# Optimization experiments

Measured on AMD Instinct MI355X. Metric: run time of the kernel, lower is better.

Reference implementation:

```python
import jax, jax.numpy as jnp
import numpy as np

A, B, D, H, O = 64, 4096, 50, 192, 3

def _xavier(key, shape, gain=0.5):
    fan_in, fan_out = shape[-1], shape[-2]
    limit = gain * np.sqrt(6.0 / (fan_in + fan_out))
    return jax.random.uniform(key, shape, jnp.float32, -limit, limit)

def setup_inputs() -> dict:
    key = jax.random.key(0)
    ks = jax.random.split(key, 12)
    return {
        "x": jax.random.normal(ks[0], (B, D), jnp.float32),
        "input_norm_weight": _xavier(ks[1], (A, D)),
        "input_norm_bias": jnp.zeros((A, D), jnp.float32),
        "layer1_weight": _xavier(ks[2], (A, H, D)),
        "layer1_bias": jnp.zeros((A, H), jnp.float32),
        "layer2_weight": _xavier(ks[3], (A, H, H)),
        "layer2_bias": jnp.zeros((A, H), jnp.float32),
        "layer3_weight": _xavier(ks[4], (A, H, H)),
        "layer3_bias": jnp.zeros((A, H), jnp.float32),
        "output_weight": _xavier(ks[5], (A, O, H)),
        "output_bias": jnp.zeros((A, O), jnp.float32),
        "skip1_weight": _xavier(ks[6], (A, H, D)),
        "skip1_bias": jnp.zeros((A, H), jnp.float32),
        "skip2_weight": _xavier(ks[7], (A, H, H)),
        "skip2_bias": jnp.zeros((A, H), jnp.float32),
        "hidden_norm_weight": _xavier(ks[8], (A, H)),
        "hidden_norm_bias": jnp.zeros((A, H), jnp.float32),
    }

def reference(x, input_norm_weight, input_norm_bias,
              layer1_weight, layer1_bias, layer2_weight, layer2_bias,
              layer3_weight, layer3_bias, output_weight, output_bias,
              skip1_weight, skip1_bias, skip2_weight, skip2_bias,
              hidden_norm_weight, hidden_norm_bias):
    # NOTE: the vectorized ensemble's "norms" are affine-only (no mean/var), per source.
    # x: [B, D] -> broadcast over agents: [A, B, D]
    x_norm = x[None, :, :] * input_norm_weight[:, None, :] + input_norm_bias[:, None, :]
    gelu = lambda t: jax.nn.gelu(t, approximate=False)  # torch F.gelu exact
    # per-agent GEMMs: [A,B,in] x [A,out,in] -> [A,B,out]
    h1 = gelu(jnp.einsum('abi,ahi->abh', x_norm, layer1_weight) + layer1_bias[:, None, :]) \
         + jnp.einsum('abi,ahi->abh', x_norm, skip1_weight) + skip1_bias[:, None, :]
    h2 = gelu(jnp.einsum('abi,ahi->abh', h1, layer2_weight) + layer2_bias[:, None, :]) \
         + jnp.einsum('abi,ahi->abh', h1, skip2_weight) + skip2_bias[:, None, :]
    h3 = jnp.einsum('abi,ahi->abh', h2, layer3_weight) + layer3_bias[:, None, :] + h2
    h3 = h3 * hidden_norm_weight[:, None, :] + hidden_norm_bias[:, None, :]
    logits = jnp.einsum('abh,aoh->abo', h3, output_weight) + output_bias[:, None, :]
    return logits  # [A, B, O]
```

## Files before the change

### kernel.cpp

```cpp
#include <hip/hip_runtime.h>
#include <math.h>

#define A_N 64
#define B_N 4096
#define D_N 50
#define H_N 192
#define O_N 3

typedef __attribute__((ext_vector_type(8))) __bf16 bf16x8;
typedef __attribute__((ext_vector_type(4))) float f32x4;

#define W1_OFF   0
#define S1_OFF   786432
#define W2_OFF   1572864
#define S2_OFF   3932160
#define W3_OFF   6291456
#define OW_OFF   8650752
#define WS_ELEMS 8847360

#if __has_builtin(__builtin_amdgcn_rcpf)
#define FRCP(x) __builtin_amdgcn_rcpf(x)
#else
#define FRCP(x) (1.0f / (x))
#endif
#if __has_builtin(__builtin_amdgcn_exp2f)
#define FEXP2(x) __builtin_amdgcn_exp2f(x)
#else
#define FEXP2(x) exp2f(x)
#endif

__device__ __forceinline__ float gelu_f(float xx) {
    float t  = 0.70710678118654752440f * xx;
    float at = fabsf(t);
    float k  = FRCP(fmaf(0.3275911f, at, 1.0f));
    float p  = fmaf(k, 1.061405429f, -1.453152027f);
    p = fmaf(k, p, 1.421413741f);
    p = fmaf(k, p, -0.284496736f);
    p = fmaf(k, p, 0.254829592f);
    p = p * k;
    float e  = FEXP2(t * t * -1.44269504088896340736f);
    float er = fmaf(-p, e, 1.0f);
    er = (t < 0.f) ? -er : er;
    return 0.5f * xx * (1.0f + er);
}

__global__ void prep_kernel(const float* __restrict__ w1, const float* __restrict__ s1,
                            const float* __restrict__ w2, const float* __restrict__ s2,
                            const float* __restrict__ w3, const float* __restrict__ ow,
                            __bf16* __restrict__ ws) {
    int idx8 = blockIdx.x * 256 + threadIdx.x;
    if (idx8 >= WS_ELEMS / 8) return;
    int idx = idx8 * 8;
    bf16x8 v;
    if (idx < W2_OFF) {
        const float* src = (idx < S1_OFF) ? w1 : s1;
        int r = (idx < S1_OFF) ? idx : idx - S1_OFF;
        int a = r / 12288;  r %= 12288;
        int nt = r / 1024;  r %= 1024;
        int ks = r / 512;   r %= 512;
        int lane = r >> 3;
        int n = nt * 16 + (lane & 15);
        int k = ks * 32 + (lane >> 4) * 8;
        const float* p = src + (size_t)(a * H_N + n) * D_N + k;
        #pragma unroll
        for (int j = 0; j < 8; ++j)
            v[j] = (k + j < D_N) ? (__bf16)p[j] : (__bf16)0.f;
    } else if (idx < OW_OFF) {
        int r = idx - W2_OFF;
        const float* src = w2;
        if (r >= 4718592)      { src = w3; r -= 4718592; }
        else if (r >= 2359296) { src = s2; r -= 2359296; }
        int a = r / 36864;  r %= 36864;
        int nt = r / 3072;  r %= 3072;
        int ks = r / 512;   r %= 512;
        int lane = r >> 3;
        int n = nt * 16 + (lane & 15);
        int k = ks * 32 + (lane >> 4) * 8;
        const float* p = src + (size_t)(a * H_N + n) * H_N + k;
        f32x4 f0 = *(const f32x4*)p;
        f32x4 f1 = *(const f32x4*)(p + 4);
        #pragma unroll
        for (int j = 0; j < 4; ++j) { v[j] = (__bf16)f0[j]; v[4 + j] = (__bf16)f1[j]; }
    } else {
        int r = idx - OW_OFF;
        int a = r / 3072;   r %= 3072;
        int ks = r / 512;   r %= 512;
        int lane = r >> 3;
        int n = lane & 15;
        int k = ks * 32 + (lane >> 4) * 8;
        if (n < O_N) {
            const float* p = ow + (size_t)(a * O_N + n) * H_N + k;
            f32x4 f0 = *(const f32x4*)p;
            f32x4 f1 = *(const f32x4*)(p + 4);
            #pragma unroll
            for (int j = 0; j < 4; ++j) { v[j] = (__bf16)f0[j]; v[4 + j] = (__bf16)f1[j]; }
        } else {
            #pragma unroll
            for (int j = 0; j < 8; ++j) v[j] = (__bf16)0.f;
        }
    }
    *(bf16x8*)(ws + idx) = v;
}

#define MFMA(a, b, c) __builtin_amdgcn_mfma_f32_16x16x32_bf16((a), (b), (c), 0, 0, 0)

__global__ __launch_bounds__(256, 2)
void srek_mfma(const float* __restrict__ x,
               const float* __restrict__ inw, const float* __restrict__ inb,
               const float* __restrict__ b1,  const float* __restrict__ b2,
               const float* __restrict__ b3,  const float* __restrict__ s1b,
               const float* __restrict__ s2b, const float* __restrict__ hnw,
               const float* __restrict__ hnb, const float* __restrict__ ob,
               const __bf16* __restrict__ ws, float* __restrict__ out) {
    __shared__ __bf16 Xs[64 * 72];
    __shared__ __bf16 Hs[64 * 200];
    __shared__ __bf16 Bs[24 * 512];

    const int bid  = blockIdx.x;
    const int slot = bid >> 3;
    const int tile = slot & 63;
    const int a    = ((bid & 7) << 3) | (slot >> 6);
    const int row0 = tile * 64;

    const int tid  = threadIdx.x;
    const int lane = tid & 63;
    const int wv   = tid >> 6;
    const int ln   = lane & 15;
    const int quad = lane >> 4;
    const int aH   = a * H_N;
    const int c0   = wv * 48;
    const int l8   = lane * 8;
    const int f6   = wv * 6;
    const int f3   = wv * 3;

    const __bf16* W1 = ws + W1_OFF + a * 12288;
    const __bf16* S1 = ws + S1_OFF + a * 12288;
    const __bf16* W2 = ws + W2_OFF + a * 36864;
    const __bf16* S2 = ws + S2_OFF + a * 36864;
    const __bf16* W3 = ws + W3_OFF + a * 36864;
    const __bf16* OWp= ws + OW_OFF + a * 3072;

    bf16x8 pf[6];
    f32x4 accT[12], accS[12], h2f[12];
    const f32x4 zero = {0.f, 0.f, 0.f, 0.f};

    #pragma unroll
    for (int i = 0; i < 6; ++i) {
        int f = f6 + i; int nt = f % 12;
        const __bf16* base = (f < 12) ? W1 : S1;
        pf[i] = *(const bf16x8*)(base + (nt * 2 + 0) * 512 + l8);
    }

    for (int e = tid; e < 64 * 64; e += 256) {
        int r = e >> 6, k = e & 63;
        float v = 0.f;
        if (k < D_N) v = x[(size_t)(row0 + r) * D_N + k] * inw[a * D_N + k] + inb[a * D_N + k];
        Xs[r * 72 + k] = (__bf16)v;
    }

    auto stage24 = [&]() {
        #pragma unroll
        for (int i = 0; i < 6; ++i) *(bf16x8*)(Bs + (f6 + i) * 512 + l8) = pf[i];
    };
    auto stage12 = [&]() {
        #pragma unroll
        for (int i = 0; i < 3; ++i) *(bf16x8*)(Bs + (f3 + i) * 512 + l8) = pf[i];
    };
    auto pf24 = [&](const __bf16* Wb, const __bf16* Sb, int KS, int ks) {
        #pragma unroll
        for (int i = 0; i < 6; ++i) {
            int f = f6 + i; int nt = f % 12;
            const __bf16* base = (f < 12) ? Wb : Sb;
            pf[i] = *(const bf16x8*)(base + (nt * KS + ks) * 512 + l8);
        }
    };
    auto pf12 = [&](int ks) {
        #pragma unroll
        for (int i = 0; i < 3; ++i)
            pf[i] = *(const bf16x8*)(W3 + ((f3 + i) * 6 + ks) * 512 + l8);
    };
    auto compute_dual = [&](const __bf16* As, int pitch, int ks) {
        bf16x8 bw[3], bs2[3];
        #pragma unroll
        for (int t = 0; t < 3; ++t) {
            bw[t]  = *(const bf16x8*)(Bs + (wv * 3 + t) * 512 + l8);
            bs2[t] = *(const bf16x8*)(Bs + (12 + wv * 3 + t) * 512 + l8);
        }
        #pragma unroll
        for (int mt = 0; mt < 4; ++mt) {
            bf16x8 av = *(const bf16x8*)(As + (mt * 16 + ln) * pitch + ks * 32 + quad * 8);
            #pragma unroll
            for (int t = 0; t < 3; ++t) {
                accT[mt * 3 + t] = MFMA(av, bw[t],  accT[mt * 3 + t]);
                accS[mt * 3 + t] = MFMA(av, bs2[t], accS[mt * 3 + t]);
            }
        }
    };
    auto compute_single = [&](int ks) {
        bf16x8 bw[3];
        #pragma unroll
        for (int t = 0; t < 3; ++t)
            bw[t] = *(const bf16x8*)(Bs + (wv * 3 + t) * 512 + l8);
        #pragma unroll
        for (int mt = 0; mt < 4; ++mt) {
            bf16x8 av = *(const bf16x8*)(Hs + (mt * 16 + ln) * 200 + ks * 32 + quad * 8);
            #pragma unroll
            for (int t = 0; t < 3; ++t)
                accT[mt * 3 + t] = MFMA(av, bw[t], accT[mt * 3 + t]);
        }
    };

    #pragma unroll
    for (int i = 0; i < 12; ++i) { accT[i] = zero; accS[i] = zero; }

    stage24();
    pf24(W1, S1, 2, 1);
    __syncthreads();
    compute_dual(Xs, 72, 0);
    __syncthreads();
    stage24();
    pf24(W2, S2, 6, 0);
    __syncthreads();
    compute_dual(Xs, 72, 1);

    #pragma unroll
    for (int t = 0; t < 3; ++t) {
        int col = c0 + t * 16 + ln;
        float bb = b1[aH + col], sb = s1b[aH + col];
        #pragma unroll
        for (int mt = 0; mt < 4; ++mt) {
            f32x4 vT = accT[mt * 3 + t], vS = accS[mt * 3 + t];
            #pragma unroll
            for (int rg = 0; rg < 4; ++rg) {
                float v = gelu_f(vT[rg] + bb) + vS[rg] + sb;
                Hs[(mt * 16 + quad * 4 + rg) * 200 + col] = (__bf16)v;
            }
        }
    }
    #pragma unroll
    for (int i = 0; i < 12; ++i) { accT[i] = zero; accS[i] = zero; }
    __syncthreads();
    stage24();
    pf24(W2, S2, 6, 1);
    __syncthreads();

    #pragma unroll 1
    for (int ks = 0; ks < 5; ++ks) {
        compute_dual(Hs, 200, ks);
        __syncthreads();
        stage24();
        if (ks < 4) pf24(W2, S2, 6, ks + 2);
        else        pf12(0);
        __syncthreads();
    }
    compute_dual(Hs, 200, 5);
    #pragma unroll
    for (int t = 0; t < 3; ++t) {
        int col = c0 + t * 16 + ln;
        float bb = b2[aH + col], sb = s2b[aH + col];
        #pragma unroll
        for (int mt = 0; mt < 4; ++mt) {
            #pragma unroll
            for (int rg = 0; rg < 4; ++rg)
                h2f[mt * 3 + t][rg] = gelu_f(accT[mt * 3 + t][rg] + bb) + accS[mt * 3 + t][rg] + sb;
        }
    }
    #pragma unroll
    for (int i = 0; i < 12; ++i) accT[i] = zero;
    __syncthreads();
    stage12();
    #pragma unroll
    for (int t = 0; t < 3; ++t) {
        int col = c0 + t * 16 + ln;
        #pragma unroll
        for (int mt = 0; mt < 4; ++mt)
            #pragma unroll
            for (int rg = 0; rg < 4; ++rg)
                Hs[(mt * 16 + quad * 4 + rg) * 200 + col] = (__bf16)h2f[mt * 3 + t][rg];
    }
    pf12(1);
    __syncthreads();

    #pragma unroll 1
    for (int ks = 0; ks < 5; ++ks) {
        compute_single(ks);
        __syncthreads();
        stage12();
        if (ks < 4) pf12(ks + 2);
        __syncthreads();
    }
    compute_single(5);

    bf16x8 owf[6];
    #pragma unroll
    for (int ks = 0; ks < 6; ++ks)
        owf[ks] = *(const bf16x8*)(OWp + ks * 512 + l8);

    #pragma unroll
    for (int t = 0; t < 3; ++t) {
        int col = c0 + t * 16 + ln;
        float b3v = b3[aH + col], nw = hnw[aH + col], nb = hnb[aH + col];
        #pragma unroll
        for (int mt = 0; mt < 4; ++mt)
            #pragma unroll
            for (int rg = 0; rg < 4; ++rg)
                h2f[mt * 3 + t][rg] = (accT[mt * 3 + t][rg] + b3v + h2f[mt * 3 + t][rg]) * nw + nb;
    }
    __syncthreads();
    #pragma unroll
    for (int t = 0; t < 3; ++t) {
        int col = c0 + t * 16 + ln;
        #pragma unroll
        for (int mt = 0; mt < 4; ++mt)
            #pragma unroll
            for (int rg = 0; rg < 4; ++rg)
                Hs[(mt * 16 + quad * 4 + rg) * 200 + col] = (__bf16)h2f[mt * 3 + t][rg];
    }
    __syncthreads();

    {
        f32x4 acco = zero;
        #pragma unroll
        for (int ks = 0; ks < 6; ++ks) {
            bf16x8 av = *(const bf16x8*)(Hs + (wv * 16 + ln) * 200 + ks * 32 + quad * 8);
            acco = MFMA(av, owf[ks], acco);
        }
        if (ln < O_N) {
            float obv = ob[a * O_N + ln];
            #pragma unroll
            for (int rg = 0; rg < 4; ++rg) {
                int r = row0 + wv * 16 + quad * 4 + rg;
                out[((size_t)a * B_N + r) * O_N + ln] = acco[rg] + obv;
            }
        }
    }
}

extern "C" void kernel_launch(void* const* d_in, const int* in_sizes, int n_in,
                              void* d_out, int out_size, void* d_ws, size_t ws_size,
                              hipStream_t stream) {
    const float* x   = (const float*)d_in[0];
    const float* inw = (const float*)d_in[1];
    const float* inb = (const float*)d_in[2];
    const float* w1  = (const float*)d_in[3];
    const float* b1  = (const float*)d_in[4];
    const float* w2  = (const float*)d_in[5];
    const float* b2  = (const float*)d_in[6];
    const float* w3  = (const float*)d_in[7];
    const float* b3  = (const float*)d_in[8];
    const float* ow  = (const float*)d_in[9];
    const float* ob  = (const float*)d_in[10];
    const float* s1w = (const float*)d_in[11];
    const float* s1b = (const float*)d_in[12];
    const float* s2w = (const float*)d_in[13];
    const float* s2b = (const float*)d_in[14];
    const float* hnw = (const float*)d_in[15];
    const float* hnb = (const float*)d_in[16];

    __bf16* ws = (__bf16*)d_ws;

    prep_kernel<<<dim3((WS_ELEMS / 8 + 255) / 256), dim3(256), 0, stream>>>(
        w1, s1w, w2, s2w, w3, ow, ws);

    srek_mfma<<<dim3(A_N * (B_N / 64)), dim3(256), 0, stream>>>(
        x, inw, inb, b1, b2, b3, s1b, s2b, hnw, hnb, ob, ws, (float*)d_out);
}
```

Before: 263.1 us.

## Load weight fragments straight to registers, drop LDS staging, transpose MFMA operands

The main kernel no longer stages weight fragments through shared memory. Each wave loads its own pre-swizzled bf16 weight fragments from global memory into registers one k-step ahead, which removes most of the per-k-step __syncthreads barriers. MFMA operands are swapped so each lane's output holds 4 consecutive columns, which allows vectorized bias loads and bf16x4 stores into shared memory. The prep kernel is rewritten to transpose tiles through shared memory with coalesced reads, and occupancy is raised to 3 blocks per CU. The trade-offs are more register pressure and repeated global weight reads by the four waves.

```diff
diff --git a/kernel.cpp b/kernel.cpp
--- a/kernel.cpp
+++ b/kernel.cpp
@@ -8,6 +8,7 @@
 #define O_N 3
 
 typedef __attribute__((ext_vector_type(8))) __bf16 bf16x8;
+typedef __attribute__((ext_vector_type(4))) __bf16 bf16x4;
 typedef __attribute__((ext_vector_type(4))) float f32x4;
 
 #define W1_OFF   0
@@ -44,67 +45,89 @@
     return 0.5f * xx * (1.0f + er);
 }
 
-__global__ void prep_kernel(const float* __restrict__ w1, const float* __restrict__ s1,
-                            const float* __restrict__ w2, const float* __restrict__ s2,
-                            const float* __restrict__ w3, const float* __restrict__ ow,
-                            __bf16* __restrict__ ws) {
-    int idx8 = blockIdx.x * 256 + threadIdx.x;
-    if (idx8 >= WS_ELEMS / 8) return;
-    int idx = idx8 * 8;
-    bf16x8 v;
-    if (idx < W2_OFF) {
-        const float* src = (idx < S1_OFF) ? w1 : s1;
-        int r = (idx < S1_OFF) ? idx : idx - S1_OFF;
-        int a = r / 12288;  r %= 12288;
-        int nt = r / 1024;  r %= 1024;
-        int ks = r / 512;   r %= 512;
-        int lane = r >> 3;
-        int n = nt * 16 + (lane & 15);
-        int k = ks * 32 + (lane >> 4) * 8;
-        const float* p = src + (size_t)(a * H_N + n) * D_N + k;
-        #pragma unroll
-        for (int j = 0; j < 8; ++j)
-            v[j] = (k + j < D_N) ? (__bf16)p[j] : (__bf16)0.f;
-    } else if (idx < OW_OFF) {
-        int r = idx - W2_OFF;
-        const float* src = w2;
-        if (r >= 4718592)      { src = w3; r -= 4718592; }
-        else if (r >= 2359296) { src = s2; r -= 2359296; }
-        int a = r / 36864;  r %= 36864;
-        int nt = r / 3072;  r %= 3072;
-        int ks = r / 512;   r %= 512;
-        int lane = r >> 3;
-        int n = nt * 16 + (lane & 15);
-        int k = ks * 32 + (lane >> 4) * 8;
-        const float* p = src + (size_t)(a * H_N + n) * H_N + k;
-        f32x4 f0 = *(const f32x4*)p;
-        f32x4 f1 = *(const f32x4*)(p + 4);
-        #pragma unroll
-        for (int j = 0; j < 4; ++j) { v[j] = (__bf16)f0[j]; v[4 + j] = (__bf16)f1[j]; }
+__global__ __launch_bounds__(256)
+void prep_kernel(const float* __restrict__ w1, const float* __restrict__ s1,
+                 const float* __restrict__ w2, const float* __restrict__ s2,
+                 const float* __restrict__ w3, const float* __restrict__ ow,
+                 __bf16* __restrict__ ws) {
+    __shared__ __bf16 T[192 * 72];
+    const int b   = blockIdx.x;
+    const int tid = threadIdx.x;
+
+    if (b < 384) {
+        int m = b / 128;
+        int r = b % 128; int a = r >> 1; int half = r & 1;
+        const float* src = ((m == 0) ? w2 : (m == 1) ? s2 : w3) + (size_t)a * 36864;
+        __bf16* dst = ws + ((m == 0) ? W2_OFF : (m == 1) ? S2_OFF : W3_OFF) + (size_t)a * 36864;
+        for (int rc = half * 3; rc < half * 3 + 3; ++rc) {
+            #pragma unroll
+            for (int i = 0; i < 6; ++i) {
+                int f4 = i * 256 + tid;
+                int row = f4 / 48, kc = (f4 % 48) * 4;
+                f32x4 v = *(const f32x4*)(src + (size_t)(rc * 32 + row) * 192 + kc);
+                bf16x4 o;
+                #pragma unroll
+                for (int j = 0; j < 4; ++j) o[j] = (__bf16)v[j];
+                *(bf16x4*)(T + row * 200 + kc) = o;
+            }
+            __syncthreads();
+            #pragma unroll
+            for (int i = 0; i < 3; ++i) {
+                int fr = i * 256 + tid;
+                int f = fr >> 6, lane = fr & 63;
+                int ntl = f / 6, ks = f % 6;
+                int n = ntl * 16 + (lane & 15), k = ks * 32 + (lane >> 4) * 8;
+                bf16x8 v = *(const bf16x8*)(T + n * 200 + k);
+                *(bf16x8*)(dst + ((size_t)(rc * 2 + ntl) * 6 + ks) * 512 + lane * 8) = v;
+            }
+            __syncthreads();
+        }
+    } else if (b < 512) {
+        int r = b - 384; int m = r >> 6; int a = r & 63;
+        const float* src = (m ? s1 : w1) + (size_t)a * 9600;
+        __bf16* dst = ws + (m ? S1_OFF : W1_OFF) + (size_t)a * 12288;
+        for (int e = tid; e < 192 * 72; e += 256) T[e] = (__bf16)0.f;
+        __syncthreads();
+        for (int e = tid; e < 9600; e += 256) {
+            int row = e / 50, k = e - row * 50;
+            T[row * 72 + k] = (__bf16)src[e];
+        }
+        __syncthreads();
+        #pragma unroll
+        for (int i = 0; i < 6; ++i) {
+            int fr = i * 256 + tid;
+            int f = fr >> 6, lane = fr & 63;
+            int nt = f >> 1, ks = f & 1;
+            int n = nt * 16 + (lane & 15), k = ks * 32 + (lane >> 4) * 8;
+            bf16x8 v = *(const bf16x8*)(T + n * 72 + k);
+            *(bf16x8*)(dst + (size_t)(nt * 2 + ks) * 512 + lane * 8) = v;
+        }
     } else {
-        int r = idx - OW_OFF;
-        int a = r / 3072;   r %= 3072;
-        int ks = r / 512;   r %= 512;
-        int lane = r >> 3;
-        int n = lane & 15;
-        int k = ks * 32 + (lane >> 4) * 8;
-        if (n < O_N) {
-            const float* p = ow + (size_t)(a * O_N + n) * H_N + k;
-            f32x4 f0 = *(const f32x4*)p;
-            f32x4 f1 = *(const f32x4*)(p + 4);
-            #pragma unroll
-            for (int j = 0; j < 4; ++j) { v[j] = (__bf16)f0[j]; v[4 + j] = (__bf16)f1[j]; }
-        } else {
-            #pragma unroll
-            for (int j = 0; j < 8; ++j) v[j] = (__bf16)0.f;
-        }
-    }
-    *(bf16x8*)(ws + idx) = v;
+        int r = b - 512;
+        #pragma unroll
+        for (int i = 0; i < 8; ++i) {
+            int fr = (r * 8 + i) * 256 + tid;
+            int a = fr / 384, rem = fr - a * 384;
+            int ks = rem >> 6, lane = rem & 63;
+            int n = lane & 15, k = ks * 32 + (lane >> 4) * 8;
+            bf16x8 v;
+            if (n < O_N) {
+                const float* p = ow + ((size_t)a * O_N + n) * H_N + k;
+                f32x4 f0 = *(const f32x4*)p, f1 = *(const f32x4*)(p + 4);
+                #pragma unroll
+                for (int j = 0; j < 4; ++j) { v[j] = (__bf16)f0[j]; v[4 + j] = (__bf16)f1[j]; }
+            } else {
+                #pragma unroll
+                for (int j = 0; j < 8; ++j) v[j] = (__bf16)0.f;
+            }
+            *(bf16x8*)(ws + OW_OFF + (size_t)a * 3072 + ks * 512 + lane * 8) = v;
+        }
+    }
 }
 
 #define MFMA(a, b, c) __builtin_amdgcn_mfma_f32_16x16x32_bf16((a), (b), (c), 0, 0, 0)
 
-__global__ __launch_bounds__(256, 2)
+__global__ __launch_bounds__(256, 3)
 void srek_mfma(const float* __restrict__ x,
                const float* __restrict__ inw, const float* __restrict__ inb,
                const float* __restrict__ b1,  const float* __restrict__ b2,
@@ -114,7 +137,6 @@
                const __bf16* __restrict__ ws, float* __restrict__ out) {
     __shared__ __bf16 Xs[64 * 72];
     __shared__ __bf16 Hs[64 * 200];
-    __shared__ __bf16 Bs[24 * 512];
 
     const int bid  = blockIdx.x;
     const int slot = bid >> 3;
@@ -130,25 +152,23 @@
     const int aH   = a * H_N;
     const int c0   = wv * 48;
     const int l8   = lane * 8;
-    const int f6   = wv * 6;
     const int f3   = wv * 3;
 
-    const __bf16* W1 = ws + W1_OFF + a * 12288;
-    const __bf16* S1 = ws + S1_OFF + a * 12288;
-    const __bf16* W2 = ws + W2_OFF + a * 36864;
-    const __bf16* S2 = ws + S2_OFF + a * 36864;
-    const __bf16* W3 = ws + W3_OFF + a * 36864;
-    const __bf16* OWp= ws + OW_OFF + a * 3072;
-
-    bf16x8 pf[6];
+    const __bf16* W1 = ws + W1_OFF + (size_t)a * 12288;
+    const __bf16* S1 = ws + S1_OFF + (size_t)a * 12288;
+    const __bf16* W2 = ws + W2_OFF + (size_t)a * 36864;
+    const __bf16* S2 = ws + S2_OFF + (size_t)a * 36864;
+    const __bf16* W3 = ws + W3_OFF + (size_t)a * 36864;
+    const __bf16* OWp= ws + OW_OFF + (size_t)a * 3072;
+
+    bf16x8 nxt[6];
     f32x4 accT[12], accS[12], h2f[12];
     const f32x4 zero = {0.f, 0.f, 0.f, 0.f};
 
     #pragma unroll
-    for (int i = 0; i < 6; ++i) {
-        int f = f6 + i; int nt = f % 12;
-        const __bf16* base = (f < 12) ? W1 : S1;
-        pf[i] = *(const bf16x8*)(base + (nt * 2 + 0) * 512 + l8);
+    for (int t = 0; t < 3; ++t) {
+        nxt[t]     = *(const bf16x8*)(W1 + ((f3 + t) * 2 + 0) * 512 + l8);
+        nxt[3 + t] = *(const bf16x8*)(S1 + ((f3 + t) * 2 + 0) * 512 + l8);
     }
 
     for (int e = tid; e < 64 * 64; e += 256) {
@@ -158,163 +178,155 @@
         Xs[r * 72 + k] = (__bf16)v;
     }
 
-    auto stage24 = [&]() {
-        #pragma unroll
-        for (int i = 0; i < 6; ++i) *(bf16x8*)(Bs + (f6 + i) * 512 + l8) = pf[i];
+    auto compute_dual = [&](const __bf16* As, int pitch, int ks,
+                            const bf16x8* cw, const bf16x8* cs) {
+        #pragma unroll
+        for (int mt = 0; mt < 4; ++mt) {
+            bf16x8 av = *(const bf16x8*)(As + (mt * 16 + ln) * pitch + ks * 32 + quad * 8);
+            #pragma unroll
+            for (int t = 0; t < 3; ++t) {
+                accT[mt * 3 + t] = MFMA(cw[t], av, accT[mt * 3 + t]);
+                accS[mt * 3 + t] = MFMA(cs[t], av, accS[mt * 3 + t]);
+            }
+        }
     };
-    auto stage12 = [&]() {
-        #pragma unroll
-        for (int i = 0; i < 3; ++i) *(bf16x8*)(Bs + (f3 + i) * 512 + l8) = pf[i];
+    auto compute_single = [&](int ks, const bf16x8* cw) {
+        #pragma unroll
+        for (int mt = 0; mt < 4; ++mt) {
+            bf16x8 av = *(const bf16x8*)(Hs + (mt * 16 + ln) * 200 + ks * 32 + quad * 8);
+            #pragma unroll
+            for (int t = 0; t < 3; ++t)
+                accT[mt * 3 + t] = MFMA(cw[t], av, accT[mt * 3 + t]);
+        }
     };
-    auto pf24 = [&](const __bf16* Wb, const __bf16* Sb, int KS, int ks) {
-        #pragma unroll
-        for (int i = 0; i < 6; ++i) {
-            int f = f6 + i; int nt = f % 12;
-            const __bf16* base = (f < 12) ? Wb : Sb;
-            pf[i] = *(const bf16x8*)(base + (nt * KS + ks) * 512 + l8);
-        }
-    };
-    auto pf12 = [&](int ks) {
-        #pragma unroll
-        for (int i = 0; i < 3; ++i)
-            pf[i] = *(const bf16x8*)(W3 + ((f3 + i) * 6 + ks) * 512 + l8);
-    };
-    auto compute_dual = [&](const __bf16* As, int pitch, int ks) {
-        bf16x8 bw[3], bs2[3];
+
+    #pragma unroll
+    for (int i = 0; i < 12; ++i) { accT[i] = zero; accS[i] = zero; }
+    __syncthreads();
+
+    {
+        bf16x8 cw[3], cs[3];
+        #pragma unroll
+        for (int t = 0; t < 3; ++t) { cw[t] = nxt[t]; cs[t] = nxt[3 + t]; }
         #pragma unroll
         for (int t = 0; t < 3; ++t) {
-            bw[t]  = *(const bf16x8*)(Bs + (wv * 3 + t) * 512 + l8);
-            bs2[t] = *(const bf16x8*)(Bs + (12 + wv * 3 + t) * 512 + l8);
-        }
-        #pragma unroll
-        for (int mt = 0; mt < 4; ++mt) {
-            bf16x8 av = *(const bf16x8*)(As + (mt * 16 + ln) * pitch + ks * 32 + quad * 8);
+            nxt[t]     = *(const bf16x8*)(W1 + ((f3 + t) * 2 + 1) * 512 + l8);
+            nxt[3 + t] = *(const bf16x8*)(S1 + ((f3 + t) * 2 + 1) * 512 + l8);
+        }
+        compute_dual(Xs, 72, 0, cw, cs);
+        #pragma unroll
+        for (int t = 0; t < 3; ++t) { cw[t] = nxt[t]; cs[t] = nxt[3 + t]; }
+        #pragma unroll
+        for (int t = 0; t < 3; ++t) {
+            nxt[t]     = *(const bf16x8*)(W2 + ((f3 + t) * 6 + 0) * 512 + l8);
+            nxt[3 + t] = *(const bf16x8*)(S2 + ((f3 + t) * 6 + 0) * 512 + l8);
+        }
+        compute_dual(Xs, 72, 1, cw, cs);
+    }
+    #pragma unroll
+    for (int t = 0; t < 3; ++t) {
+        int colb = c0 + t * 16 + quad * 4;
+        f32x4 bb = *(const f32x4*)(b1 + aH + colb);
+        f32x4 sb = *(const f32x4*)(s1b + aH + colb);
+        #pragma unroll
+        for (int mt = 0; mt < 4; ++mt) {
+            bf16x4 o;
+            #pragma unroll
+            for (int rg = 0; rg < 4; ++rg)
+                o[rg] = (__bf16)(gelu_f(accT[mt * 3 + t][rg] + bb[rg]) + accS[mt * 3 + t][rg] + sb[rg]);
+            *(bf16x4*)(Hs + (mt * 16 + ln) * 200 + colb) = o;
+        }
+    }
+    #pragma unroll
+    for (int i = 0; i < 12; ++i) { accT[i] = zero; accS[i] = zero; }
+    __syncthreads();
+
+    #pragma unroll
+    for (int ks = 0; ks < 6; ++ks) {
+        bf16x8 cw[3], cs[3];
+        #pragma unroll
+        for (int t = 0; t < 3; ++t) { cw[t] = nxt[t]; cs[t] = nxt[3 + t]; }
+        if (ks < 5) {
             #pragma unroll
             for (int t = 0; t < 3; ++t) {
-                accT[mt * 3 + t] = MFMA(av, bw[t],  accT[mt * 3 + t]);
-                accS[mt * 3 + t] = MFMA(av, bs2[t], accS[mt * 3 + t]);
-            }
-        }
-    };
-    auto compute_single = [&](int ks) {
-        bf16x8 bw[3];
-        #pragma unroll
-        for (int t = 0; t < 3; ++t)
-            bw[t] = *(const bf16x8*)(Bs + (wv * 3 + t) * 512 + l8);
-        #pragma unroll
-        for (int mt = 0; mt < 4; ++mt) {
-            bf16x8 av = *(const bf16x8*)(Hs + (mt * 16 + ln) * 200 + ks * 32 + quad * 8);
+                nxt[t]     = *(const bf16x8*)(W2 + ((f3 + t) * 6 + ks + 1) * 512 + l8);
+                nxt[3 + t] = *(const bf16x8*)(S2 + ((f3 + t) * 6 + ks + 1) * 512 + l8);
+            }
+        } else {
             #pragma unroll
             for (int t = 0; t < 3; ++t)
-                accT[mt * 3 + t] = MFMA(av, bw[t], accT[mt * 3 + t]);
-        }
-    };
-
-    #pragma unroll
-    for (int i = 0; i < 12; ++i) { accT[i] = zero; accS[i] = zero; }
-
-    stage24();
-    pf24(W1, S1, 2, 1);
-    __syncthreads();
-    compute_dual(Xs, 72, 0);
-    __syncthreads();
-    stage24();
-    pf24(W2, S2, 6, 0);
-    __syncthreads();
-    compute_dual(Xs, 72, 1);
-
-    #pragma unroll
-    for (int t = 0; t < 3; ++t) {
-        int col = c0 + t * 16 + ln;
-        float bb = b1[aH + col], sb = s1b[aH + col];
-        #pragma unroll
-        for (int mt = 0; mt < 4; ++mt) {
-            f32x4 vT = accT[mt * 3 + t], vS = accS[mt * 3 + t];
-            #pragma unroll
-            for (int rg = 0; rg < 4; ++rg) {
-                float v = gelu_f(vT[rg] + bb) + vS[rg] + sb;
-                Hs[(mt * 16 + quad * 4 + rg) * 200 + col] = (__bf16)v;
-            }
-        }
-    }
-    #pragma unroll
-    for (int i = 0; i < 12; ++i) { accT[i] = zero; accS[i] = zero; }
-    __syncthreads();
-    stage24();
-    pf24(W2, S2, 6, 1);
-    __syncthreads();
-
-    #pragma unroll 1
-    for (int ks = 0; ks < 5; ++ks) {
-        compute_dual(Hs, 200, ks);
-        __syncthreads();
-        stage24();
-        if (ks < 4) pf24(W2, S2, 6, ks + 2);
-        else        pf12(0);
-        __syncthreads();
-    }
-    compute_dual(Hs, 200, 5);
-    #pragma unroll
-    for (int t = 0; t < 3; ++t) {
-        int col = c0 + t * 16 + ln;
-        float bb = b2[aH + col], sb = s2b[aH + col];
-        #pragma unroll
-        for (int mt = 0; mt < 4; ++mt) {
+                nxt[t] = *(const bf16x8*)(W3 + ((f3 + t) * 6 + 0) * 512 + l8);
+        }
+        compute_dual(Hs, 200, ks, cw, cs);
+    }
+    #pragma unroll
+    for (int t = 0; t < 3; ++t) {
+        int colb = c0 + t * 16 + quad * 4;
+        f32x4 bb = *(const f32x4*)(b2 + aH + colb);
+        f32x4 sb = *(const f32x4*)(s2b + aH + colb);
+        #pragma unroll
+        for (int mt = 0; mt < 4; ++mt)
             #pragma unroll
             for (int rg = 0; rg < 4; ++rg)
-                h2f[mt * 3 + t][rg] = gelu_f(accT[mt * 3 + t][rg] + bb) + accS[mt * 3 + t][rg] + sb;
-        }
+                h2f[mt * 3 + t][rg] = gelu_f(accT[mt * 3 + t][rg] + bb[rg]) + accS[mt * 3 + t][rg] + sb[rg];
     }
     #pragma unroll
     for (int i = 0; i < 12; ++i) accT[i] = zero;
     __syncthreads();
-    stage12();
-    #pragma unroll
-    for (int t = 0; t < 3; ++t) {
-        int col = c0 + t * 16 + ln;
+    #pragma unroll
+    for (int t = 0; t < 3; ++t) {
+        int colb = c0 + t * 16 + quad * 4;
+        #pragma unroll
+        for (int mt = 0; mt < 4; ++mt) {
+            bf16x4 o;
+            #pragma unroll
+            for (int rg = 0; rg < 4; ++rg) o[rg] = (__bf16)h2f[mt * 3 + t][rg];
+            *(bf16x4*)(Hs + (mt * 16 + ln) * 200 + colb) = o;
+        }
+    }
+    __syncthreads();
+
+    bf16x8 ow6[6];
+    #pragma unroll
+    for (int ks = 0; ks < 6; ++ks) {
+        bf16x8 cw[3];
+        #pragma unroll
+        for (int t = 0; t < 3; ++t) cw[t] = nxt[t];
+        if (ks < 5) {
+            #pragma unroll
+            for (int t = 0; t < 3; ++t)
+                nxt[t] = *(const bf16x8*)(W3 + ((f3 + t) * 6 + ks + 1) * 512 + l8);
+        } else {
+            #pragma unroll
+            for (int kk = 0; kk < 6; ++kk)
+                ow6[kk] = *(const bf16x8*)(OWp + kk * 512 + l8);
+        }
+        compute_single(ks, cw);
+    }
+    #pragma unroll
+    for (int t = 0; t < 3; ++t) {
+        int colb = c0 + t * 16 + quad * 4;
+        f32x4 b3v = *(const f32x4*)(b3  + aH + colb);
+        f32x4 nwv = *(const f32x4*)(hnw + aH + colb);
+        f32x4 nbv = *(const f32x4*)(hnb + aH + colb);
         #pragma unroll
         for (int mt = 0; mt < 4; ++mt)
             #pragma unroll
             for (int rg = 0; rg < 4; ++rg)
-                Hs[(mt * 16 + quad * 4 + rg) * 200 + col] = (__bf16)h2f[mt * 3 + t][rg];
-    }
-    pf12(1);
-    __syncthreads();
-
-    #pragma unroll 1
-    for (int ks = 0; ks < 5; ++ks) {
-        compute_single(ks);
-        __syncthreads();
-        stage12();
-        if (ks < 4) pf12(ks + 2);
-        __syncthreads();
-    }
-    compute_single(5);
-
-    bf16x8 owf[6];
-    #pragma unroll
-    for (int ks = 0; ks < 6; ++ks)
-        owf[ks] = *(const bf16x8*)(OWp + ks * 512 + l8);
-
-    #pragma unroll
-    for (int t = 0; t < 3; ++t) {
-        int col = c0 + t * 16 + ln;
-        float b3v = b3[aH + col], nw = hnw[aH + col], nb = hnb[aH + col];
-        #pragma unroll
-        for (int mt = 0; mt < 4; ++mt)
-            #pragma unroll
-            for (int rg = 0; rg < 4; ++rg)
-                h2f[mt * 3 + t][rg] = (accT[mt * 3 + t][rg] + b3v + h2f[mt * 3 + t][rg]) * nw + nb;
-    }
-    __syncthreads();
-    #pragma unroll
-    for (int t = 0; t < 3; ++t) {
-        int col = c0 + t * 16 + ln;
-        #pragma unroll
-        for (int mt = 0; mt < 4; ++mt)
-            #pragma unroll
-            for (int rg = 0; rg < 4; ++rg)
-                Hs[(mt * 16 + quad * 4 + rg) * 200 + col] = (__bf16)h2f[mt * 3 + t][rg];
+                h2f[mt * 3 + t][rg] = fmaf(accT[mt * 3 + t][rg] + b3v[rg] + h2f[mt * 3 + t][rg],
+                                           nwv[rg], nbv[rg]);
+    }
+    __syncthreads();
+    #pragma unroll
+    for (int t = 0; t < 3; ++t) {
+        int colb = c0 + t * 16 + quad * 4;
+        #pragma unroll
+        for (int mt = 0; mt < 4; ++mt) {
+            bf16x4 o;
+            #pragma unroll
+            for (int rg = 0; rg < 4; ++rg) o[rg] = (__bf16)h2f[mt * 3 + t][rg];
+            *(bf16x4*)(Hs + (mt * 16 + ln) * 200 + colb) = o;
+        }
     }
     __syncthreads();
 
@@ -323,15 +335,13 @@
         #pragma unroll
         for (int ks = 0; ks < 6; ++ks) {
             bf16x8 av = *(const bf16x8*)(Hs + (wv * 16 + ln) * 200 + ks * 32 + quad * 8);
-            acco = MFMA(av, owf[ks], acco);
-        }
-        if (ln < O_N) {
-            float obv = ob[a * O_N + ln];
-            #pragma unroll
-            for (int rg = 0; rg < 4; ++rg) {
-                int r = row0 + wv * 16 + quad * 4 + rg;
-                out[((size_t)a * B_N + r) * O_N + ln] = acco[rg] + obv;
-            }
+            acco = MFMA(ow6[ks], av, acco);
+        }
+        if (quad == 0) {
+            float* po = out + ((size_t)a * B_N + row0 + wv * 16 + ln) * O_N;
+            po[0] = acco[0] + ob[a * O_N + 0];
+            po[1] = acco[1] + ob[a * O_N + 1];
+            po[2] = acco[2] + ob[a * O_N + 2];
         }
     }
 }
@@ -359,8 +369,7 @@
 
     __bf16* ws = (__bf16*)d_ws;
 
-    prep_kernel<<<dim3((WS_ELEMS / 8 + 255) / 256), dim3(256), 0, stream>>>(
-        w1, s1w, w2, s2w, w3, ow, ws);
+    prep_kernel<<<dim3(524), dim3(256), 0, stream>>>(w1, s1w, w2, s2w, w3, ow, ws);
 
     srek_mfma<<<dim3(A_N * (B_N / 64)), dim3(256), 0, stream>>>(
         x, inw, inb, b1, b2, b3, s1b, s2b, hnw, hnb, ob, ws, (float*)d_out);
```

After: 246.5 us. 6.3% less time.
